# Kernel tuning notes

Measured on AMD Instinct MI355X. Metric: run time of the kernel, lower is better.

## Reference

```python
import jax, jax.numpy as jnp
import numpy as np

B, C, H, W = 16, 1536, 32, 32
M = 64      # num_clusters
L = 128     # cluster_dim
G = 256     # token_dim
HID = 512
OT_ITERS = 3
EPS = 1e-6


def setup_inputs() -> dict:
    key = jax.random.key(0)
    ks = jax.random.split(key, 12)
    def w(k, shape, fan_in):
        return jax.random.normal(k, shape, jnp.float32) * (1.0 / np.sqrt(fan_in))
    return {
        'x': jax.random.normal(ks[0], (B, C, H, W), jnp.float32),
        't': jax.random.normal(ks[1], (B, C), jnp.float32),
        # token_features: Linear(C->512), ReLU, Linear(512->G)
        'Wt1': w(ks[2], (HID, C), C), 'bt1': jnp.zeros((HID,), jnp.float32),
        'Wt2': w(ks[3], (G, HID), HID), 'bt2': jnp.zeros((G,), jnp.float32),
        # cluster_features: 1x1 Conv(C->512), ReLU, 1x1 Conv(512->L)
        'Wc1': w(ks[4], (HID, C), C), 'bc1': jnp.zeros((HID,), jnp.float32),
        'Wc2': w(ks[5], (L, HID), HID), 'bc2': jnp.zeros((L,), jnp.float32),
        # score: 1x1 Conv(C->512), ReLU, 1x1 Conv(512->M)
        'Ws1': w(ks[6], (HID, C), C), 'bs1': jnp.zeros((HID,), jnp.float32),
        'Ws2': w(ks[7], (M, HID), HID), 'bs2': jnp.zeros((M,), jnp.float32),
        # temp_predictor: Conv1d(L->1, k=1)
        'Wtp': w(ks[8], (L,), L), 'btp': jnp.zeros((), jnp.float32),
        'dust_bin': jnp.asarray(1.0, jnp.float32),
        'burst_b': jnp.asarray(0.0, jnp.float32),
        'burst_p': jnp.asarray(1.0, jnp.float32),
        'lambda_discount': jnp.asarray(0.5, jnp.float32),
    }


def _log_optimal_transport(scores, alpha, iters):
    # scores: [B, m, n]; alpha: scalar dust-bin logit
    b, m, n = scores.shape
    Z0 = jnp.concatenate([scores, jnp.broadcast_to(alpha, (b, 1, n))], axis=1)  # [B, m+1, n]
    norm = -jnp.log(jnp.asarray(m + n, scores.dtype))
    log_mu = jnp.concatenate([jnp.full((m,), norm, scores.dtype),
                              (jnp.log(jnp.asarray(n, scores.dtype)) + norm)[None]])  # [m+1]
    log_nu = jnp.full((n,), norm, scores.dtype)
    u = jnp.zeros((b, m + 1), scores.dtype)
    v = jnp.zeros((b, n), scores.dtype)
    for _ in range(iters):
        u = log_mu - jax.nn.logsumexp(Z0 + v[:, None, :], axis=2)
        v = log_nu - jax.nn.logsumexp(Z0 + u[:, :, None], axis=1)
    return Z0 + u[:, :, None] + v[:, None, :] - norm


def _l2norm(a, axis):
    return a / jnp.maximum(jnp.linalg.norm(a, axis=axis, keepdims=True), 1e-12)


def _forward(x, t, Wt1, bt1, Wt2, bt2, Wc1, bc1, Wc2, bc2, Ws1, bs1, Ws2, bs2,
             Wtp, btp, dust_bin, burst_b, burst_p, lambda_discount):
    b, c, h, w = x.shape
    n = h * w
    xf = x.reshape(b, c, n)  # [B, C, N] (1x1 convs == per-pixel MLP)
    # cluster features f: [B, L, N]
    h1 = jax.nn.relu(jnp.einsum('bcn,oc->bon', xf, Wc1) + bc1[:, None])
    f = jnp.einsum('bhn,lh->bln', h1, Wc2) + bc2[:, None]
    # assignment scores p: [B, M, N]
    h2 = jax.nn.relu(jnp.einsum('bcn,oc->bon', xf, Ws1) + bs1[:, None])
    p = jnp.einsum('bhn,mh->bmn', h2, Ws2) + bs2[:, None]
    # global token: [B, G]
    tok = jax.nn.relu(t @ Wt1.T + bt1) @ Wt2.T + bt2
    # Sinkhorn OT soft assignment, drop dust bin row
    P = jnp.exp(_log_optimal_transport(p, dust_bin, OT_ITERS))[:, :-1, :]  # [B, M, N]
    # burst-aware weighting
    f_norm = _l2norm(f, axis=1)                                  # [B, L, N]
    T_i = jax.nn.softplus(jnp.einsum('bln,l->bn', f, Wtp) + btp)  # [B, N]
    sim = jnp.einsum('bli,blj->bij', f_norm, f_norm)              # [B, N, N]
    T_avg = (T_i[:, :, None] + T_i[:, None, :]) * 0.5
    burst_w = jax.nn.sigmoid(T_avg * sim + burst_b)
    discount = jnp.clip(jnp.sum(burst_w, axis=-1) ** burst_p, 1e-3, 1e3)  # [B, N]
    lam = jax.nn.sigmoid(lambda_discount)
    P_adj = (1.0 - lam) * P + lam * (P / (discount[:, None, :] + EPS))
    # local aggregation: (f[:, :, None, :] * P[:, None, :, :]).sum(-1) == batched matmul
    agg = jnp.einsum('bln,bmn->blm', f, P_adj)  # [B, L, M]
    agg = _l2norm(agg, axis=1).reshape(b, -1)   # [B, L*M]
    tok_n = _l2norm(tok, axis=-1)
    g = jnp.concatenate([tok_n, agg], axis=-1)  # [B, G + L*M]
    return _l2norm(g, axis=-1)


def reference(x, t, Wt1, bt1, Wt2, bt2, Wc1, bc1, Wc2, bc2, Ws1, bs1, Ws2, bs2,
              Wtp, btp, dust_bin, burst_b, burst_p, lambda_discount):
    return _forward(x, t, Wt1, bt1, Wt2, bt2, Wc1, bc1, Wc2, bc2, Ws1, bs1, Ws2, bs2,
                    Wtp, btp, dust_bin, burst_b, burst_p, lambda_discount)
```

## Files before the change

### kernel.cpp

```cpp
#include <hip/hip_runtime.h>
#include <math.h>

#define B_   16
#define C_   1536
#define N_   1024
#define M_   64
#define L_   128
#define G_   256
#define HID_ 512

typedef __attribute__((ext_vector_type(8))) short short8;
typedef __attribute__((ext_vector_type(4))) float floatx4;

__device__ __forceinline__ unsigned short f2bf_rne(float x) {
    unsigned u = __float_as_uint(x);
    unsigned r = u + 0x7fffu + ((u >> 16) & 1u);
    return (unsigned short)(r >> 16);
}
__device__ __forceinline__ unsigned pack_bf2(float lo, float hi) {
    unsigned a = __float_as_uint(lo) + 0x8000u;
    unsigned b = __float_as_uint(hi) + 0x8000u;
    return (a >> 16) | (b & 0xffff0000u);
}

__device__ __forceinline__ void gl2lds16(const void* g, void* l) {
    __builtin_amdgcn_global_load_lds(
        (const __attribute__((address_space(1))) void*)g,
        (__attribute__((address_space(3))) void*)l, 16, 0, 0);
}

__global__ __launch_bounds__(256) void cast_w_kernel(
    const float* __restrict__ Wc1, const float* __restrict__ Ws1,
    const float* __restrict__ Wc2, const float* __restrict__ Ws2,
    unsigned short* __restrict__ Wbf, unsigned short* __restrict__ W2)
{
    const int T1 = 1024 * 1536;
    int idx = blockIdx.x * 256 + threadIdx.x;
    if (idx < T1) {
        float v = (idx < 512 * 1536) ? Wc1[idx] : Ws1[idx - 512 * 1536];
        Wbf[idx] = f2bf_rne(v);
    } else if (idx < T1 + 192 * 1024) {
        int i2 = idx - T1;
        int row = i2 >> 10, k = i2 & 1023;
        float v = 0.f;
        if (row < 128) { if (k < 512) v = Wc2[row * 512 + k]; }
        else           { if (k >= 512) v = Ws2[(row - 128) * 512 + (k - 512)]; }
        W2[i2] = f2bf_rne(v);
    }
}

__global__ __launch_bounds__(256) void xt_kernel(
    const float* __restrict__ x, unsigned short* __restrict__ xT)
{
    __shared__ float Xs[64][65];
    const int t = threadIdx.x;
    const int n0 = blockIdx.x * 64, c0 = blockIdx.y * 64, b = blockIdx.z;
    const float* xb = x + (long)b * C_ * N_;
    #pragma unroll
    for (int it = 0; it < 16; ++it) {
        int idx = it * 256 + t, cr = idx >> 6, nc = idx & 63;
        Xs[cr][nc] = xb[(long)(c0 + cr) * N_ + n0 + nc];
    }
    __syncthreads();
    unsigned* xo = (unsigned*)(xT + (long)b * N_ * C_);
    #pragma unroll
    for (int it = 0; it < 8; ++it) {
        int idx = it * 256 + t, nr = idx >> 5, pc = idx & 31;
        xo[(long)(n0 + nr) * 768 + (c0 >> 1) + pc] =
            pack_bf2(Xs[2 * pc][nr], Xs[2 * pc + 1][nr]);
    }
}

#define G1_STAGE_A(kt, q)                                                    \
    gl2lds16(aSrc + (long)(q) * (32 * C_) + (kt) * 64,                       \
             (char*)g1lds + (((kt) & 1) * 65536 + (q) * 8192) + sdst)
#define G1_STAGE_B(kt, q)                                                    \
    gl2lds16(bSrc + (long)(q) * (32 * C_) + (kt) * 64,                       \
             (char*)g1lds + (((kt) & 1) * 65536 + 32768 + (q) * 8192) + sdst)

#define G1_PHASE(q, STAGES, TAIL)                                            \
  {                                                                          \
    const char* ab = cb + aFB + (q) * 8192;                                  \
    short8 a0 = *(const short8*)(ab + ks0);                                  \
    short8 a1 = *(const short8*)(ab + ks1);                                  \
    short8 a2 = *(const short8*)(ab + 2048 + ks0);                           \
    short8 a3 = *(const short8*)(ab + 2048 + ks1);                           \
    STAGES                                                                   \
    __builtin_amdgcn_s_barrier();                                            \
    asm volatile("s_waitcnt lgkmcnt(0)" ::: "memory");                       \
    __builtin_amdgcn_sched_barrier(0);                                       \
    __builtin_amdgcn_s_setprio(1);                                           \
    _Pragma("unroll")                                                        \
    for (int fj = 0; fj < 4; ++fj) {                                         \
      acc[2*(q)][fj]   = __builtin_amdgcn_mfma_f32_16x16x32_bf16(            \
          a0, bfr[fj][0], acc[2*(q)][fj], 0, 0, 0);                          \
      acc[2*(q)][fj]   = __builtin_amdgcn_mfma_f32_16x16x32_bf16(            \
          a1, bfr[fj][1], acc[2*(q)][fj], 0, 0, 0);                          \
      acc[2*(q)+1][fj] = __builtin_amdgcn_mfma_f32_16x16x32_bf16(            \
          a2, bfr[fj][0], acc[2*(q)+1][fj], 0, 0, 0);                        \
      acc[2*(q)+1][fj] = __builtin_amdgcn_mfma_f32_16x16x32_bf16(            \
          a3, bfr[fj][1], acc[2*(q)+1][fj], 0, 0, 0);                        \
    }                                                                        \
    __builtin_amdgcn_s_setprio(0);                                           \
    TAIL                                                                     \
    __builtin_amdgcn_s_barrier();                                            \
    __builtin_amdgcn_sched_barrier(0);                                       \
  }

#define G1_TILE(tt, S1, S2, TAIL3)                                           \
  {                                                                          \
    const char* cb = (const char*)g1lds + ((tt) & 1) * 65536;                \
    _Pragma("unroll")                                                        \
    for (int fj = 0; fj < 4; ++fj) {                                         \
      const char* bb = cb + bFB + (fj >> 1) * 8192 + (fj & 1) * 2048;        \
      bfr[fj][0] = *(const short8*)(bb + ks0);                               \
      bfr[fj][1] = *(const short8*)(bb + ks1);                               \
    }                                                                        \
    G1_PHASE(0, if (S1) { G1_STAGE_A((tt)+1, 2); G1_STAGE_A((tt)+1, 3); }, ) \
    G1_PHASE(1, if (S2) { G1_STAGE_B((tt)+2, 0); G1_STAGE_B((tt)+2, 1); }, ) \
    G1_PHASE(2, if (S2) { G1_STAGE_B((tt)+2, 2); G1_STAGE_B((tt)+2, 3); }, ) \
    G1_PHASE(3, if (S2) { G1_STAGE_A((tt)+2, 0); G1_STAGE_A((tt)+2, 1); }, TAIL3) \
  }

__global__ __launch_bounds__(512, 2) void gemm1_kernel(
    const unsigned short* __restrict__ Wbf, const unsigned short* __restrict__ xT,
    const float* __restrict__ bc1, const float* __restrict__ bs1,
    unsigned short* __restrict__ hT)
{
    __shared__ unsigned short g1lds[65536];
    const int t = threadIdx.x;
    const int lane = t & 63, w = t >> 6;
    const int n0 = blockIdx.x * 256, o0 = blockIdx.y * 256, b = blockIdx.z;

    const int sgrow = ((t & 256) ? 128 : 0) + ((t >> 3) & 31);
    const int sdst  = t * 16;
    const int sslot = ((t & 7) ^ ((t >> 3) & 7)) * 8;
    const unsigned short* aSrc = Wbf + (long)(o0 + sgrow) * C_ + sslot;
    const unsigned short* bSrc = xT + (long)b * N_ * C_
                               + (long)(n0 + sgrow) * C_ + sslot;

    const int lrow = lane & 15, kgrp = lane >> 4;
    const int wo = (w >> 2) * 128, wn = (w & 3) * 64;
    const int aFB = (w >> 2) * 4096 + lrow * 128;
    const int bFB = 32768 + ((w >> 1) & 1) * 4096 + (w & 1) * 16384 + lrow * 128;
    const int ks0 = (kgrp ^ (lrow & 7)) * 16;
    const int ks1 = ((4 + kgrp) ^ (lrow & 7)) * 16;

    floatx4 acc[8][4];
    #pragma unroll
    for (int i = 0; i < 8; ++i)
        #pragma unroll
        for (int j = 0; j < 4; ++j) acc[i][j] = (floatx4)0.0f;
    short8 bfr[4][2];

    #pragma unroll
    for (int q = 0; q < 4; ++q) { G1_STAGE_A(0, q); G1_STAGE_B(0, q); }
    #pragma unroll
    for (int q = 0; q < 4; ++q) G1_STAGE_B(1, q);
    G1_STAGE_A(1, 0); G1_STAGE_A(1, 1);
    asm volatile("s_waitcnt vmcnt(6)" ::: "memory");
    __builtin_amdgcn_s_barrier();
    __builtin_amdgcn_sched_barrier(0);

    #pragma unroll 2
    for (int t8 = 0; t8 < 22; ++t8)
        G1_TILE(t8, 1, 1, asm volatile("s_waitcnt vmcnt(6)" ::: "memory");)
    G1_TILE(22, 1, 0, asm volatile("s_waitcnt vmcnt(0)" ::: "memory");)
    G1_TILE(23, 0, 0, )

    const float* bias = (o0 < 512) ? bc1 : bs1;
    const int ob = (o0 < 512) ? o0 : o0 - 512;
    #pragma unroll
    for (int fi = 0; fi < 8; ++fi) {
        const int orow = wo + fi * 16 + kgrp * 4;
        float4 bv = *(const float4*)&bias[ob + orow];
        #pragma unroll
        for (int fj = 0; fj < 4; ++fj) {
            const int n = n0 + wn + fj * 16 + lrow;
            float v0 = fmaxf(acc[fi][fj][0] + bv.x, 0.f);
            float v1 = fmaxf(acc[fi][fj][1] + bv.y, 0.f);
            float v2 = fmaxf(acc[fi][fj][2] + bv.z, 0.f);
            float v3 = fmaxf(acc[fi][fj][3] + bv.w, 0.f);
            uint2 pk;
            pk.x = ((unsigned)f2bf_rne(v0)) | (((unsigned)f2bf_rne(v1)) << 16);
            pk.y = ((unsigned)f2bf_rne(v2)) | (((unsigned)f2bf_rne(v3)) << 16);
            *(uint2*)&hT[((long)b * N_ + n) * 1024 + o0 + orow] = pk;
        }
    }
}

__global__ __launch_bounds__(256, 2) void gemm23_kernel(
    const unsigned short* __restrict__ W2, const unsigned short* __restrict__ hT,
    const float* __restrict__ bc2, const float* __restrict__ bs2,
    float* __restrict__ f, float* __restrict__ p)
{
    __shared__ unsigned short As[64 * 32];
    __shared__ unsigned short Bs[128 * 32];
    const int t = threadIdx.x;
    const int lane = t & 63, w = t >> 6;
    const int n0 = blockIdx.x * 128, o0 = blockIdx.y * 64, b = blockIdx.z;
    const unsigned short* hTb = hT + (long)b * N_ * 1024;

    const int wo = (w >> 1) * 32, wn = (w & 1) * 64;
    const int lrow = lane & 15, kgrp = lane >> 4;
    const int arow = t >> 2, acol = (t & 3) * 8;

    floatx4 acc[2][4];
    #pragma unroll
    for (int i = 0; i < 2; ++i)
        #pragma unroll
        for (int j = 0; j < 4; ++j) acc[i][j] = (floatx4)0.0f;

    for (int k0 = 0; k0 < 1024; k0 += 32) {
        gl2lds16(W2 + (long)(o0 + arow) * 1024 + k0 + acol, (char*)As + t * 16);
        #pragma unroll
        for (int r = 0; r < 2; ++r)
            gl2lds16(hTb + (long)(n0 + r * 64 + arow) * 1024 + k0 + acol,
                     (char*)Bs + r * 4096 + t * 16);
        __syncthreads();
        short8 af[2], bfr[4];
        #pragma unroll
        for (int i = 0; i < 2; ++i)
            af[i] = *(const short8*)((const char*)As +
                        (wo + i * 16 + lrow) * 64 + kgrp * 16);
        #pragma unroll
        for (int j = 0; j < 4; ++j)
            bfr[j] = *(const short8*)((const char*)Bs +
                        (wn + j * 16 + lrow) * 64 + kgrp * 16);
        #pragma unroll
        for (int i = 0; i < 2; ++i)
            #pragma unroll
            for (int j = 0; j < 4; ++j)
                acc[i][j] = __builtin_amdgcn_mfma_f32_16x16x32_bf16(
                    af[i], bfr[j], acc[i][j], 0, 0, 0);
        __syncthreads();
    }

    #pragma unroll
    for (int i = 0; i < 2; ++i) {
        int o = o0 + wo + i * 16 + kgrp * 4;
        #pragma unroll
        for (int j = 0; j < 4; ++j) {
            int n = n0 + wn + j * 16 + lrow;
            #pragma unroll
            for (int r = 0; r < 4; ++r) {
                int oo = o + r;
                float v = acc[i][j][r];
                if (oo < 128) f[((long)b * L_ + oo) * N_ + n] = v + bc2[oo];
                else p[((long)b * M_ + (oo - 128)) * N_ + n] = v + bs2[oo - 128];
            }
        }
    }
}

__global__ __launch_bounds__(256) void token1_kernel(
    const float* __restrict__ t_in, const float* __restrict__ Wt1,
    const float* __restrict__ bt1, float* __restrict__ hid)
{
    const int lane = threadIdx.x & 63, w = threadIdx.x >> 6;
    const int o = blockIdx.x * 4 + w, b = blockIdx.y;
    const float4* wr = (const float4*)(Wt1 + (long)o * C_);
    const float4* tb = (const float4*)(t_in + (long)b * C_);
    float acc = 0.f;
    #pragma unroll
    for (int i = 0; i < 6; ++i) {
        float4 a = wr[i * 64 + lane], tv = tb[i * 64 + lane];
        acc += a.x * tv.x + a.y * tv.y + a.z * tv.z + a.w * tv.w;
    }
    #pragma unroll
    for (int off = 1; off < 64; off <<= 1) acc += __shfl_xor(acc, off);
    if (lane == 0) hid[b * HID_ + o] = fmaxf(acc + bt1[o], 0.f);
}

__global__ __launch_bounds__(256) void token2_kernel(
    const float* __restrict__ hid, const float* __restrict__ Wt2,
    const float* __restrict__ bt2, float* __restrict__ tok)
{
    const int lane = threadIdx.x & 63, w = threadIdx.x >> 6;
    const int g = blockIdx.x * 4 + w, b = blockIdx.y;
    const float4* wr = (const float4*)(Wt2 + (long)g * HID_);
    const float4* hb = (const float4*)(hid + (long)b * HID_);
    float acc = 0.f;
    #pragma unroll
    for (int i = 0; i < 2; ++i) {
        float4 a = wr[i * 64 + lane], hv = hb[i * 64 + lane];
        acc += a.x * hv.x + a.y * hv.y + a.z * hv.z + a.w * hv.w;
    }
    #pragma unroll
    for (int off = 1; off < 64; off <<= 1) acc += __shfl_xor(acc, off);
    if (lane == 0) tok[b * G_ + g] = acc + bt2[g];
}

__global__ __launch_bounds__(256) void token3_kernel(
    const float* __restrict__ tok, float* __restrict__ tokn)
{
    __shared__ float red[4];
    const int b = blockIdx.x, t = threadIdx.x;
    float v = tok[b * G_ + t];
    float ss = v * v;
    #pragma unroll
    for (int off = 1; off < 64; off <<= 1) ss += __shfl_xor(ss, off);
    if ((t & 63) == 0) red[t >> 6] = ss;
    __syncthreads();
    float inv = 1.f / fmaxf(sqrtf(red[0] + red[1] + red[2] + red[3]), 1e-12f);
    tokn[b * G_ + t] = v * inv;
}

template<bool FIRST>
__global__ __launch_bounds__(256) void ku_kernel(
    float* __restrict__ p, const float* __restrict__ dust,
    const float* __restrict__ bvec, float* __restrict__ avec)
{
    const int t = threadIdx.x, lane = t & 63, w = t >> 6;
    const int m = blockIdx.x * 4 + w, b = blockIdx.y;
    if (m > M_) return;
    const float* bv = bvec + b * N_;
    float s = 0.f;
    if (m < M_) {
        float* row = p + ((long)b * M_ + m) * N_;
        #pragma unroll
        for (int i = 0; i < 16; ++i) {
            int n = i * 64 + lane;
            if (FIRST) {
                float K = expf(row[n]);
                row[n] = K;
                s += K;
            } else {
                s += row[n] * bv[n];
            }
        }
    } else {
        float ea = expf(dust[0]);
        if (FIRST) s = 16.f * ea;
        else {
            #pragma unroll
            for (int i = 0; i < 16; ++i) s += bv[i * 64 + lane];
            s *= ea;
        }
    }
    #pragma unroll
    for (int off = 1; off < 64; off <<= 1) s += __shfl_xor(s, off);
    if (lane == 0) {
        float mu = (m < M_) ? (1.f / 1088.f) : (1024.f / 1088.f);
        avec[b * (M_ + 1) + m] = mu / s;
    }
}

__global__ __launch_bounds__(256) void kv_kernel(
    const float* __restrict__ K, const float* __restrict__ dust,
    const float* __restrict__ avec, float* __restrict__ bvec)
{
    __shared__ float a_s[M_ + 1];
    const int t = threadIdx.x, b = blockIdx.y;
    const int n = blockIdx.x * 256 + t;
    if (t < M_ + 1) a_s[t] = avec[b * (M_ + 1) + t];
    __syncthreads();
    float s = expf(dust[0]) * a_s[M_];
    const float* col = K + (long)b * M_ * N_ + n;
    #pragma unroll
    for (int m = 0; m < M_; ++m) s = fmaf(col[(long)m * N_], a_s[m], s);
    bvec[b * N_ + n] = (1.f / 1088.f) / s;
}

__global__ __launch_bounds__(256) void tnorm_kernel(
    const float* __restrict__ f, const float* __restrict__ Wtp,
    const float* __restrict__ btp, unsigned short* __restrict__ fnT,
    float* __restrict__ T, float* __restrict__ draw)
{
    __shared__ float Ft[L_][65];
    __shared__ float invs[64];
    __shared__ float wtp_s[L_];
    const int b = blockIdx.y, n0 = blockIdx.x * 64, t = threadIdx.x;
    const float* fb = f + (long)b * L_ * N_;

    if (t < L_) wtp_s[t] = Wtp[t];
    for (int it = 0; it < 32; ++it) {
        int idx = it * 256 + t;
        int l = idx >> 6, c = idx & 63;
        Ft[l][c] = fb[(long)l * N_ + n0 + c];
    }
    __syncthreads();
    if (t < 64) {
        float ss = 0.f, dot = 0.f;
        #pragma unroll
        for (int l = 0; l < L_; ++l) {
            float v = Ft[l][t];
            ss = fmaf(v, v, ss);
            dot = fmaf(v, wtp_s[l], dot);
        }
        invs[t] = 1.f / fmaxf(sqrtf(ss), 1e-12f);
        float xx = dot + btp[0];
        T[b * N_ + n0 + t] = (xx > 0.f) ? (xx + log1pf(expf(-xx)))
                                        : log1pf(expf(xx));
        draw[b * N_ + n0 + t] = 0.f;
    }
    __syncthreads();
    unsigned* fo = (unsigned*)fnT;
    for (int it = 0; it < 16; ++it) {
        int idx = it * 256 + t;
        int nl = idx >> 6, jp = idx & 63;
        float inv = invs[nl];
        fo[(((long)b * N_ + n0 + nl) << 6) + jp] =
            pack_bf2(Ft[2 * jp][nl] * inv, Ft[2 * jp + 1][nl] * inv);
    }
}

__global__ __launch_bounds__(256) void sim_kernel(
    const unsigned short* __restrict__ fnT, const float* __restrict__ T,
    const float* __restrict__ bb, float* __restrict__ draw)
{
    __shared__ unsigned short As[64 * 136];
    __shared__ unsigned short Bs[64 * 136];
    __shared__ float Ti[64], Tj[64];
    const int b = blockIdx.z, i0 = blockIdx.y * 64, j0base = blockIdx.x * 256;
    const int t = threadIdx.x, lane = t & 63, w = t >> 6;
    const int lrow = lane & 15, kgrp = lane >> 4;
    const unsigned short* fb = fnT + (long)b * N_ * 128;
    const float burstb = bb[0];

    if (t < 64) Ti[t] = T[b * N_ + i0 + t];
    const int srow = t >> 4, scol = (t & 15) * 8;
    #pragma unroll
    for (int r = 0; r < 4; ++r) {
        uint4 av = *(const uint4*)(fb + (long)(i0 + r * 16 + srow) * 128 + scol);
        *(uint4*)((char*)As + (r * 16 + srow) * 272 + scol * 2) = av;
    }

    float rs[4] = {0.f, 0.f, 0.f, 0.f};
    for (int jj = 0; jj < 4; ++jj) {
        const int j0 = j0base + jj * 64;
        __syncthreads();
        #pragma unroll
        for (int r = 0; r < 4; ++r) {
            uint4 bv = *(const uint4*)(fb + (long)(j0 + r * 16 + srow) * 128 + scol);
            *(uint4*)((char*)Bs + (r * 16 + srow) * 272 + scol * 2) = bv;
        }
        if (t >= 64 && t < 128) Tj[t - 64] = T[b * N_ + j0 + (t - 64)];
        __syncthreads();

        floatx4 acc[4];
        #pragma unroll
        for (int j = 0; j < 4; ++j) acc[j] = (floatx4)0.0f;
        #pragma unroll
        for (int k0 = 0; k0 < 128; k0 += 32) {
            short8 af = *(const short8*)((const char*)As +
                            (w * 16 + lrow) * 272 + k0 * 2 + kgrp * 16);
            #pragma unroll
            for (int j = 0; j < 4; ++j) {
                short8 bf = *(const short8*)((const char*)Bs +
                                (j * 16 + lrow) * 272 + k0 * 2 + kgrp * 16);
                acc[j] = __builtin_amdgcn_mfma_f32_16x16x32_bf16(af, bf, acc[j], 0, 0, 0);
            }
        }
        #pragma unroll
        for (int j = 0; j < 4; ++j) {
            float Tjv = Tj[j * 16 + lrow];
            #pragma unroll
            for (int r = 0; r < 4; ++r) {
                float Tiv = Ti[w * 16 + kgrp * 4 + r];
                float xarg = 0.5f * (Tiv + Tjv) * acc[j][r] + burstb;
                rs[r] += 1.f / (1.f + expf(-xarg));
            }
        }
    }

    #pragma unroll
    for (int off = 1; off < 16; off <<= 1)
        #pragma unroll
        for (int r = 0; r < 4; ++r) rs[r] += __shfl_xor(rs[r], off);
    if (lrow == 0) {
        #pragma unroll
        for (int r = 0; r < 4; ++r)
            atomicAdd(&draw[b * N_ + i0 + w * 16 + kgrp * 4 + r], rs[r]);
    }
}

__global__ __launch_bounds__(256) void wn_kernel(
    const float* __restrict__ draw, const float* __restrict__ bp,
    const float* __restrict__ lamd, float* __restrict__ wn,
    float* __restrict__ agg)
{
    const int id = blockIdx.x * 256 + threadIdx.x;
    float d = powf(draw[id], bp[0]);
    d = fminf(fmaxf(d, 1e-3f), 1e3f);
    float lam = 1.f / (1.f + expf(-lamd[0]));
    wn[id] = (1.f - lam) + lam / (d + 1e-6f);
    for (int i = id; i < B_ * L_ * M_; i += B_ * N_) agg[i] = 0.f;
}

__global__ __launch_bounds__(256) void agg_kernel(
    const float* __restrict__ f, const float* __restrict__ Kmat,
    const float* __restrict__ avec, const float* __restrict__ dust,
    const float* __restrict__ wn, float* __restrict__ agg)
{
    __shared__ float fch[L_][65];
    __shared__ float Pch[M_][65];
    __shared__ float a_s[M_ + 1], cf[64];
    const int b = blockIdx.y, n0 = blockIdx.x * 64;
    const int t = threadIdx.x, tx = t & 15, ty = t >> 4;
    const float* fb = f + (long)b * L_ * N_;
    const float* Kb = Kmat + (long)b * M_ * N_;

    if (t < M_ + 1) a_s[t] = avec[b * (M_ + 1) + t];
    __syncthreads();

    for (int idx = t; idx < L_ * 64; idx += 256) {
        int l = idx >> 6, c = idx & 63;
        fch[l][c] = fb[(long)l * N_ + n0 + c];
    }
    for (int idx = t; idx < M_ * 64; idx += 256) {
        int m = idx >> 6, c = idx & 63;
        Pch[m][c] = Kb[(long)m * N_ + n0 + c] * a_s[m];
    }
    __syncthreads();

    if (t < 64) {
        float s = expf(dust[0]) * a_s[M_];
        #pragma unroll
        for (int m = 0; m < M_; ++m) s += Pch[m][t];
        cf[t] = wn[b * N_ + n0 + t] / s;
    }
    __syncthreads();

    float acc[8][4] = {};
    for (int n = 0; n < 64; ++n) {
        float cfn = cf[n];
        float fv[8], pv[4];
        #pragma unroll
        for (int i = 0; i < 8; ++i) fv[i] = fch[ty + 16 * i][n];
        #pragma unroll
        for (int j = 0; j < 4; ++j) pv[j] = Pch[tx * 4 + j][n] * cfn;
        #pragma unroll
        for (int i = 0; i < 8; ++i)
            #pragma unroll
            for (int j = 0; j < 4; ++j)
                acc[i][j] = fmaf(fv[i], pv[j], acc[i][j]);
    }
    #pragma unroll
    for (int i = 0; i < 8; ++i)
        #pragma unroll
        for (int j = 0; j < 4; ++j)
            atomicAdd(&agg[((long)b * L_ + (ty + 16 * i)) * M_ + tx * 4 + j],
                      acc[i][j]);
}

__global__ __launch_bounds__(256) void final_kernel(
    const float* __restrict__ tokn, const float* __restrict__ agg,
    float* __restrict__ out)
{
    __shared__ float invm[M_];
    __shared__ float red[4];
    __shared__ float s_invtot;
    const int b = blockIdx.x, t = threadIdx.x;
    const float* ab = agg + (long)b * L_ * M_;

    if (t < 64) {
        float ss = 0.f;
        for (int l = 0; l < L_; ++l) {
            float v = ab[l * M_ + t];
            ss = fmaf(v, v, ss);
        }
        invm[t] = 1.f / fmaxf(sqrtf(ss), 1e-12f);
    }
    __syncthreads();

    float part;
    {
        float tn = tokn[b * G_ + t];
        part = tn * tn;
    }
    for (int idx = t; idx < L_ * M_; idx += 256) {
        float v = ab[idx] * invm[idx & 63];
        part = fmaf(v, v, part);
    }
    for (int off = 32; off; off >>= 1) part += __shfl_down(part, off);
    if ((t & 63) == 0) red[t >> 6] = part;
    __syncthreads();
    if (t == 0)
        s_invtot = 1.f / fmaxf(sqrtf(red[0] + red[1] + red[2] + red[3]), 1e-12f);
    __syncthreads();

    const float invtot = s_invtot;
    float* ob = out + (long)b * (G_ + L_ * M_);
    ob[t] = tokn[b * G_ + t] * invtot;
    for (int idx = t; idx < L_ * M_; idx += 256)
        ob[G_ + idx] = ab[idx] * invm[idx & 63] * invtot;
}

extern "C" void kernel_launch(void* const* d_in, const int* in_sizes, int n_in,
                              void* d_out, int out_size, void* d_ws, size_t ws_size,
                              hipStream_t stream)
{
    const float* x    = (const float*)d_in[0];
    const float* t_in = (const float*)d_in[1];
    const float* Wt1  = (const float*)d_in[2];
    const float* bt1  = (const float*)d_in[3];
    const float* Wt2  = (const float*)d_in[4];
    const float* bt2  = (const float*)d_in[5];
    const float* Wc1  = (const float*)d_in[6];
    const float* bc1  = (const float*)d_in[7];
    const float* Wc2  = (const float*)d_in[8];
    const float* bc2  = (const float*)d_in[9];
    const float* Ws1  = (const float*)d_in[10];
    const float* bs1  = (const float*)d_in[11];
    const float* Ws2  = (const float*)d_in[12];
    const float* bs2  = (const float*)d_in[13];
    const float* Wtp  = (const float*)d_in[14];
    const float* btp  = (const float*)d_in[15];
    const float* dust = (const float*)d_in[16];
    const float* bb   = (const float*)d_in[17];
    const float* bp   = (const float*)d_in[18];
    const float* lamd = (const float*)d_in[19];

    char* wsb = (char*)d_ws;
    unsigned short* xT  = (unsigned short*)wsb;
    float* f    = (float*)(wsb + 0);
    float* p    = (float*)(wsb + 8388608);
    unsigned short* fnT = (unsigned short*)(wsb + 12582912);
    float* hid  = (float*)(wsb + 16777216);
    float* tok  = (float*)(wsb + 16809984);
    float* tokn = (float*)(wsb + 16826368);
    float* T    = (float*)(wsb + 16842752);
    float* draw = (float*)(wsb + 16908288);
    float* wgt  = (float*)(wsb + 16973824);
    float* agg  = (float*)(wsb + 17039360);
    float* avec = (float*)(wsb + 17563648);
    float* bvec = (float*)(wsb + 17567808);
    unsigned short* hT  = (unsigned short*)(wsb + 50331648);
    unsigned short* Wbf = (unsigned short*)(wsb + 83886080);
    unsigned short* W2  = (unsigned short*)(wsb + 87031808);
    float* out  = (float*)d_out;

    cast_w_kernel<<<6912, 256, 0, stream>>>(Wc1, Ws1, Wc2, Ws2, Wbf, W2);

    xt_kernel   <<<dim3(16, 24, 16), 256, 0, stream>>>(x, xT);
    gemm1_kernel<<<dim3(4, 4, 16), 512, 0, stream>>>(Wbf, xT, bc1, bs1, hT);
    gemm23_kernel<<<dim3(8, 3, 16), 256, 0, stream>>>(W2, hT, bc2, bs2, f, p);

    token1_kernel<<<dim3(128, 16), 256, 0, stream>>>(t_in, Wt1, bt1, hid);
    token2_kernel<<<dim3(64, 16), 256, 0, stream>>>(hid, Wt2, bt2, tok);
    token3_kernel<<<16, 256, 0, stream>>>(tok, tokn);

    ku_kernel<true> <<<dim3(17, 16), 256, 0, stream>>>(p, dust, bvec, avec);
    kv_kernel       <<<dim3(4, 16), 256, 0, stream>>>(p, dust, avec, bvec);
    ku_kernel<false><<<dim3(17, 16), 256, 0, stream>>>(p, dust, bvec, avec);
    kv_kernel       <<<dim3(4, 16), 256, 0, stream>>>(p, dust, avec, bvec);
    ku_kernel<false><<<dim3(17, 16), 256, 0, stream>>>(p, dust, bvec, avec);

    tnorm_kernel<<<dim3(16, 16), 256, 0, stream>>>(f, Wtp, btp, fnT, T, draw);
    sim_kernel  <<<dim3(4, 16, 16), 256, 0, stream>>>(fnT, T, bb, draw);
    wn_kernel   <<<64, 256, 0, stream>>>(draw, bp, lamd, wgt, agg);
    agg_kernel  <<<dim3(16, 16), 256, 0, stream>>>(f, p, avec, dust, wgt, agg);
    final_kernel<<<16, 256, 0, stream>>>(tokn, agg, out);
}
```

Measured before the change: 376.4 us.

## Fuse Sinkhorn iterations into one kernel, halve gemm23 K range, prefetch sim tiles

Replaces the five separate ku/kv launches with a single per-batch 1024-thread kernel that keeps the row and column scaling vectors in shared memory across iterations. This removes launch overhead and global round trips, but only 16 blocks are resident. gemm23 now reads only the half of the hidden dimension matching its output group (cluster vs score branch), which skips the block-diagonal zeros of the combined weight. sim_kernel register-prefetches the next B tile and raises wave priority around the MFMA loop.

```diff
diff --git a/kernel.cpp b/kernel.cpp
--- a/kernel.cpp
+++ b/kernel.cpp
@@ -204,6 +204,7 @@
     const int wo = (w >> 1) * 32, wn = (w & 1) * 64;
     const int lrow = lane & 15, kgrp = lane >> 4;
     const int arow = t >> 2, acol = (t & 3) * 8;
+    const int klo = (o0 < 128) ? 0 : 512;
 
     floatx4 acc[2][4];
     #pragma unroll
@@ -211,11 +212,11 @@
         #pragma unroll
         for (int j = 0; j < 4; ++j) acc[i][j] = (floatx4)0.0f;
 
-    for (int k0 = 0; k0 < 1024; k0 += 32) {
-        gl2lds16(W2 + (long)(o0 + arow) * 1024 + k0 + acol, (char*)As + t * 16);
+    for (int k0 = 0; k0 < 512; k0 += 32) {
+        gl2lds16(W2 + (long)(o0 + arow) * 1024 + klo + k0 + acol, (char*)As + t * 16);
         #pragma unroll
         for (int r = 0; r < 2; ++r)
-            gl2lds16(hTb + (long)(n0 + r * 64 + arow) * 1024 + k0 + acol,
+            gl2lds16(hTb + (long)(n0 + r * 64 + arow) * 1024 + klo + k0 + acol,
                      (char*)Bs + r * 4096 + t * 16);
         __syncthreads();
         short8 af[2], bfr[4];
@@ -306,60 +307,75 @@
     tokn[b * G_ + t] = v * inv;
 }
 
-template<bool FIRST>
-__global__ __launch_bounds__(256) void ku_kernel(
+__global__ __launch_bounds__(1024) void sinkhorn_kernel(
     float* __restrict__ p, const float* __restrict__ dust,
-    const float* __restrict__ bvec, float* __restrict__ avec)
-{
+    float* __restrict__ avec)
+{
+    __shared__ float a_s[M_ + 1];
+    __shared__ float b_s[N_];
+    __shared__ float bsum_red[16];
+    const int b = blockIdx.x;
     const int t = threadIdx.x, lane = t & 63, w = t >> 6;
-    const int m = blockIdx.x * 4 + w, b = blockIdx.y;
-    if (m > M_) return;
-    const float* bv = bvec + b * N_;
-    float s = 0.f;
-    if (m < M_) {
-        float* row = p + ((long)b * M_ + m) * N_;
+    float* K = p + (long)b * M_ * N_;
+    const float ed = expf(dust[0]);
+
+    #pragma unroll
+    for (int r = 0; r < 4; ++r) {
+        const int m = w * 4 + r;
+        float* row = K + (long)m * N_;
+        float s = 0.f;
         #pragma unroll
         for (int i = 0; i < 16; ++i) {
             int n = i * 64 + lane;
-            if (FIRST) {
-                float K = expf(row[n]);
-                row[n] = K;
-                s += K;
-            } else {
-                s += row[n] * bv[n];
+            float Kv = expf(row[n]);
+            row[n] = Kv;
+            s += Kv;
+        }
+        #pragma unroll
+        for (int off = 1; off < 64; off <<= 1) s += __shfl_xor(s, off);
+        if (lane == 0) a_s[m] = (1.f / 1088.f) / s;
+    }
+    if (t == 0) a_s[M_] = (1.f / 1088.f) / ed;
+    __syncthreads();
+
+    for (int iter = 0; iter < 2; ++iter) {
+        {
+            float s = ed * a_s[M_];
+            const float* col = K + t;
+            #pragma unroll
+            for (int m = 0; m < M_; ++m) s = fmaf(col[(long)m * N_], a_s[m], s);
+            float bn = (1.f / 1088.f) / s;
+            b_s[t] = bn;
+            float ss = bn;
+            #pragma unroll
+            for (int off = 1; off < 64; off <<= 1) ss += __shfl_xor(ss, off);
+            if (lane == 0) bsum_red[w] = ss;
+        }
+        __syncthreads();
+        #pragma unroll
+        for (int r = 0; r < 4; ++r) {
+            const int m = w * 4 + r;
+            const float* row = K + (long)m * N_;
+            float s = 0.f;
+            #pragma unroll
+            for (int i = 0; i < 16; ++i) {
+                int n = i * 64 + lane;
+                s = fmaf(row[n], b_s[n], s);
             }
-        }
-    } else {
-        float ea = expf(dust[0]);
-        if (FIRST) s = 16.f * ea;
-        else {
-            #pragma unroll
-            for (int i = 0; i < 16; ++i) s += bv[i * 64 + lane];
-            s *= ea;
-        }
-    }
-    #pragma unroll
-    for (int off = 1; off < 64; off <<= 1) s += __shfl_xor(s, off);
-    if (lane == 0) {
-        float mu = (m < M_) ? (1.f / 1088.f) : (1024.f / 1088.f);
-        avec[b * (M_ + 1) + m] = mu / s;
-    }
-}
-
-__global__ __launch_bounds__(256) void kv_kernel(
-    const float* __restrict__ K, const float* __restrict__ dust,
-    const float* __restrict__ avec, float* __restrict__ bvec)
-{
-    __shared__ float a_s[M_ + 1];
-    const int t = threadIdx.x, b = blockIdx.y;
-    const int n = blockIdx.x * 256 + t;
-    if (t < M_ + 1) a_s[t] = avec[b * (M_ + 1) + t];
-    __syncthreads();
-    float s = expf(dust[0]) * a_s[M_];
-    const float* col = K + (long)b * M_ * N_ + n;
-    #pragma unroll
-    for (int m = 0; m < M_; ++m) s = fmaf(col[(long)m * N_], a_s[m], s);
-    bvec[b * N_ + n] = (1.f / 1088.f) / s;
+            #pragma unroll
+            for (int off = 1; off < 64; off <<= 1) s += __shfl_xor(s, off);
+            if (lane == 0) a_s[m] = (1.f / 1088.f) / s;
+        }
+        if (t == 0) {
+            float bs = 0.f;
+            #pragma unroll
+            for (int i = 0; i < 16; ++i) bs += bsum_red[i];
+            a_s[M_] = (1024.f / 1088.f) / (ed * bs);
+        }
+        __syncthreads();
+    }
+
+    if (t < M_ + 1) avec[b * (M_ + 1) + t] = a_s[t];
 }
 
 __global__ __launch_bounds__(256) void tnorm_kernel(
@@ -425,22 +441,31 @@
         uint4 av = *(const uint4*)(fb + (long)(i0 + r * 16 + srow) * 128 + scol);
         *(uint4*)((char*)As + (r * 16 + srow) * 272 + scol * 2) = av;
     }
+    uint4 bv[4];
+    #pragma unroll
+    for (int r = 0; r < 4; ++r)
+        bv[r] = *(const uint4*)(fb + (long)(j0base + r * 16 + srow) * 128 + scol);
 
     float rs[4] = {0.f, 0.f, 0.f, 0.f};
+    #pragma unroll
     for (int jj = 0; jj < 4; ++jj) {
-        const int j0 = j0base + jj * 64;
         __syncthreads();
         #pragma unroll
-        for (int r = 0; r < 4; ++r) {
-            uint4 bv = *(const uint4*)(fb + (long)(j0 + r * 16 + srow) * 128 + scol);
-            *(uint4*)((char*)Bs + (r * 16 + srow) * 272 + scol * 2) = bv;
-        }
-        if (t >= 64 && t < 128) Tj[t - 64] = T[b * N_ + j0 + (t - 64)];
+        for (int r = 0; r < 4; ++r)
+            *(uint4*)((char*)Bs + (r * 16 + srow) * 272 + scol * 2) = bv[r];
+        if (t >= 64 && t < 128) Tj[t - 64] = T[b * N_ + j0base + jj * 64 + (t - 64)];
+        if (jj < 3) {
+            #pragma unroll
+            for (int r = 0; r < 4; ++r)
+                bv[r] = *(const uint4*)(fb +
+                    (long)(j0base + (jj + 1) * 64 + r * 16 + srow) * 128 + scol);
+        }
         __syncthreads();
 
         floatx4 acc[4];
         #pragma unroll
         for (int j = 0; j < 4; ++j) acc[j] = (floatx4)0.0f;
+        __builtin_amdgcn_s_setprio(1);
         #pragma unroll
         for (int k0 = 0; k0 < 128; k0 += 32) {
             short8 af = *(const short8*)((const char*)As +
@@ -452,6 +477,7 @@
                 acc[j] = __builtin_amdgcn_mfma_f32_16x16x32_bf16(af, bf, acc[j], 0, 0, 0);
             }
         }
+        __builtin_amdgcn_s_setprio(0);
         #pragma unroll
         for (int j = 0; j < 4; ++j) {
             float Tjv = Tj[j * 16 + lrow];
@@ -625,7 +651,6 @@
     float* wgt  = (float*)(wsb + 16973824);
     float* agg  = (float*)(wsb + 17039360);
     float* avec = (float*)(wsb + 17563648);
-    float* bvec = (float*)(wsb + 17567808);
     unsigned short* hT  = (unsigned short*)(wsb + 50331648);
     unsigned short* Wbf = (unsigned short*)(wsb + 83886080);
     unsigned short* W2  = (unsigned short*)(wsb + 87031808);
@@ -641,11 +666,7 @@
     token2_kernel<<<dim3(64, 16), 256, 0, stream>>>(hid, Wt2, bt2, tok);
     token3_kernel<<<16, 256, 0, stream>>>(tok, tokn);
 
-    ku_kernel<true> <<<dim3(17, 16), 256, 0, stream>>>(p, dust, bvec, avec);
-    kv_kernel       <<<dim3(4, 16), 256, 0, stream>>>(p, dust, avec, bvec);
-    ku_kernel<false><<<dim3(17, 16), 256, 0, stream>>>(p, dust, bvec, avec);
-    kv_kernel       <<<dim3(4, 16), 256, 0, stream>>>(p, dust, avec, bvec);
-    ku_kernel<false><<<dim3(17, 16), 256, 0, stream>>>(p, dust, bvec, avec);
+    sinkhorn_kernel<<<16, 1024, 0, stream>>>(p, dust, avec);
 
     tnorm_kernel<<<dim3(16, 16), 256, 0, stream>>>(f, Wtp, btp, fnT, T, draw);
     sim_kernel  <<<dim3(4, 16, 16), 256, 0, stream>>>(fnT, T, bb, draw);
```

Result: slower. 433.0 us (+15.0%).
